# Kernel optimization log

Measured on AMD Instinct MI355X. Metric: run time of the kernel, lower is better.

Reference implementation:

```python
import jax, jax.numpy as jnp
import numpy as np

DIM = 2048
N_HEADS = 32
N_KV_HEADS = 8
HEAD_DIM = DIM // N_HEADS
ROPE_BASE = 10000.0
BATCH = 2
SEQ = 2048


def _rope_cos_sin(seq_len, dtype=jnp.float32):
    inv_freq = 1.0 / (ROPE_BASE ** (jnp.arange(0, HEAD_DIM, 2, dtype=jnp.float32) / HEAD_DIM))
    pos = jnp.arange(seq_len, dtype=jnp.float32)
    freqs = pos[:, None] * inv_freq[None, :]  # (seq, head_dim/2)
    return jnp.cos(freqs).astype(dtype), jnp.sin(freqs).astype(dtype)


def _apply_rope(x, cos, sin):
    # x: (b, h, s, d); cos/sin: (s, d/2). Interleaved (even/odd) RoPE.
    cos = cos[None, None, :, :]
    sin = sin[None, None, :, :]
    x_even = x[..., ::2]
    x_odd = x[..., 1::2]
    rot_even = x_even * cos - x_odd * sin
    rot_odd = x_even * sin + x_odd * cos
    out = jnp.stack((rot_even, rot_odd), axis=-1)
    return out.reshape(x.shape)


def setup_inputs() -> dict:
    key = jax.random.key(0)
    ks = jax.random.split(key, 5)
    s = 0.02
    return {
        "x": jax.random.normal(ks[0], (BATCH, SEQ, DIM), dtype=jnp.float32),
        "wq": jax.random.normal(ks[1], (DIM, N_HEADS * HEAD_DIM), dtype=jnp.float32) * s,
        "wk": jax.random.normal(ks[2], (DIM, N_KV_HEADS * HEAD_DIM), dtype=jnp.float32) * s,
        "wv": jax.random.normal(ks[3], (DIM, N_KV_HEADS * HEAD_DIM), dtype=jnp.float32) * s,
        "wo": jax.random.normal(ks[4], (DIM, DIM), dtype=jnp.float32) * s,
    }


def reference(x, wq, wk, wv, wo):
    b, s, _ = x.shape
    q = (x @ wq).reshape(b, s, N_HEADS, HEAD_DIM).transpose(0, 2, 1, 3)
    k = (x @ wk).reshape(b, s, N_KV_HEADS, HEAD_DIM).transpose(0, 2, 1, 3)
    v = (x @ wv).reshape(b, s, N_KV_HEADS, HEAD_DIM).transpose(0, 2, 1, 3)
    cos, sin = _rope_cos_sin(s, x.dtype)
    q = _apply_rope(q, cos, sin)
    k = _apply_rope(k, cos, sin)
    rep = N_HEADS // N_KV_HEADS
    if rep > 1:
        k = jnp.repeat(k, rep, axis=1)
        v = jnp.repeat(v, rep, axis=1)
    scores = jnp.einsum("bhqd,bhkd->bhqk", q, k) / (HEAD_DIM ** 0.5)
    causal = jnp.tril(jnp.ones((s, s), dtype=bool))
    scores = jnp.where(causal[None, None], scores, -jnp.inf)
    probs = jax.nn.softmax(scores, axis=-1)
    out = jnp.einsum("bhqk,bhkd->bhqd", probs, v)
    out = out.transpose(0, 2, 1, 3).reshape(b, s, DIM)
    return out @ wo
```

## Files before the change

### kernel.cpp

```cpp
#include <hip/hip_runtime.h>
#include <stdint.h>

#define DIM   2048
#define NH    32
#define NKV   8
#define HD    64
#define BATCH 2
#define SEQ   2048

typedef __attribute__((ext_vector_type(8))) short  short8;
typedef __attribute__((ext_vector_type(4))) short  short4v;
typedef __attribute__((ext_vector_type(4))) float  f32x4;

#if __has_builtin(__builtin_amdgcn_exp2f)
#define EXP2(x) __builtin_amdgcn_exp2f(x)
#else
#define EXP2(x) exp2f(x)
#endif

static __device__ __forceinline__ short f2bf(float f) {
  union { float f; uint32_t u; } v; v.f = f;
  uint32_t r = v.u + 0x7FFFu + ((v.u >> 16) & 1u);
  return (short)(r >> 16);
}

static __device__ __forceinline__ uint32_t cvtpk_bf16(float lo, float hi) {
  uint32_t r;
  asm("v_cvt_pk_bf16_f32 %0, %1, %2" : "=v"(r) : "v"(lo), "v"(hi));
  return r;
}

#define GLD16(gp, lp) __builtin_amdgcn_global_load_lds(                      \
    (__attribute__((address_space(1))) void*)(void*)(gp),                    \
    (__attribute__((address_space(3))) void*)(lp), 16, 0, 0)

#define QSCALE 0.1803368801111244f


__global__ void cvt_x_kernel(const float* __restrict__ in, short* __restrict__ out, int n4) {
  int i = blockIdx.x * blockDim.x + threadIdx.x;
  if (i < n4) {
    f32x4 v = *reinterpret_cast<const f32x4*>(in + (size_t)i * 4);
    short4v o;
    o.x = f2bf(v.x); o.y = f2bf(v.y); o.z = f2bf(v.z); o.w = f2bf(v.w);
    *reinterpret_cast<short4v*>(out + (size_t)i * 4) = o;
  }
}

__global__ void transpose_bf_kernel(const float* __restrict__ in, short* __restrict__ out,
                                    int R, int C) {
  __shared__ float t[32][33];
  int c0 = blockIdx.x * 32, r0 = blockIdx.y * 32;
  int tx = threadIdx.x, ty = threadIdx.y;
#pragma unroll
  for (int j = 0; j < 32; j += 8)
    t[ty + j][tx] = in[(size_t)(r0 + ty + j) * C + c0 + tx];
  __syncthreads();
#pragma unroll
  for (int j = 0; j < 32; j += 8)
    out[(size_t)(c0 + ty + j) * R + r0 + tx] = f2bf(t[tx][ty + j]);
}

__global__ void rope_tab_kernel(float* __restrict__ ct, float* __restrict__ st) {
  int i = blockIdx.x * blockDim.x + threadIdx.x;
  if (i < SEQ * 32) {
    int pos = i >> 5, f = i & 31;
    float inv = powf(10000.0f, -(float)f / 32.0f);
    float th = (float)pos * inv;
    ct[i] = cosf(th);
    st[i] = sinf(th);
  }
}


template <int BM, int BN, int WN>
__device__ __forceinline__ void gemm_8ph(const short* __restrict__ A,
                                         const short* __restrict__ Bt,
                                         int m0, int n0,
                                         short* __restrict__ As,
                                         short* __restrict__ Bs,
                                         f32x4 (&acc)[BM / ((8 / WN) * 16)][BN / (WN * 16)]) {
  constexpr int WM = 8 / WN;
  constexpr int MREP = BM / (WM * 16);
  constexpr int NREP = BN / (WN * 16);
  constexpr int MR2 = MREP / 2, NR2 = NREP / 2;
  constexpr int APASS = BM / 64, BPASS = BN / 64;
  constexpr int ABUF = BM * 64, BBUF = BN * 64;
  constexpr int NT = DIM / 64;

  const int tid = threadIdx.x;
  const int w = tid >> 6, l = tid & 63;
  const int lg = l >> 4, lr = l & 15;
  const int wr = w / WN, wc = w % WN;
  const int srow = tid >> 3;
  const int su2 = (tid & 7) ^ (srow & 7);
  const short* pA0 = A + (size_t)(m0 + srow) * DIM + su2 * 8;
  const short* pB0 = Bt + (size_t)(n0 + srow) * DIM + su2 * 8;

  auto stageA = [&](int t, int buf) {
#pragma unroll
    for (int p = 0; p < APASS; ++p)
      GLD16(pA0 + (size_t)p * 64 * DIM + t * 64, As + buf * ABUF + p * 4096 + w * 512);
  };
  auto stageB = [&](int t, int buf) {
#pragma unroll
    for (int p = 0; p < BPASS; ++p)
      GLD16(pB0 + (size_t)p * 64 * DIM + t * 64, Bs + buf * BBUF + p * 4096 + w * 512);
  };

  short8 af[MR2][2], bf0[NR2][2], bf1[NR2][2];

  auto readA = [&](int mh, const short* base) {
#pragma unroll
    for (int i = 0; i < MR2; ++i) {
      const int row = wr * (MREP * 16) + (mh * MR2 + i) * 16 + lr;
#pragma unroll
      for (int kk = 0; kk < 2; ++kk)
        af[i][kk] = *(const short8*)&base[row * 64 + (((kk * 4 + lg) ^ (row & 7)) << 3)];
    }
  };
  auto readB = [&](short8 (&bf)[NR2][2], int nh, const short* base) {
#pragma unroll
    for (int j = 0; j < NR2; ++j) {
      const int row = wc * (NREP * 16) + (nh * NR2 + j) * 16 + lr;
#pragma unroll
      for (int kk = 0; kk < 2; ++kk)
        bf[j][kk] = *(const short8*)&base[row * 64 + (((kk * 4 + lg) ^ (row & 7)) << 3)];
    }
  };
  auto mmaQ = [&](short8 (&bf)[NR2][2], int mh, int nh) {
    __builtin_amdgcn_s_setprio(1);
#pragma unroll
    for (int i = 0; i < MR2; ++i)
#pragma unroll
      for (int j = 0; j < NR2; ++j)
#pragma unroll
        for (int kk = 0; kk < 2; ++kk)
          acc[mh * MR2 + i][nh * NR2 + j] = __builtin_amdgcn_mfma_f32_16x16x32_bf16(
              af[i][kk], bf[j][kk], acc[mh * MR2 + i][nh * NR2 + j], 0, 0, 0);
    __builtin_amdgcn_s_setprio(0);
  };

#define PH_SYNC do { __builtin_amdgcn_s_barrier();                           \
    asm volatile("s_waitcnt lgkmcnt(0)" ::: "memory");                       \
    __builtin_amdgcn_sched_barrier(0); } while (0)

  stageA(0, 0);
  stageB(0, 0);
  asm volatile("s_waitcnt vmcnt(0)" ::: "memory");
  __builtin_amdgcn_s_barrier();

  for (int t = 0; t < NT; ++t) {
    const int cur = t & 1;
    const short* ab = As + cur * ABUF;
    const short* bb = Bs + cur * BBUF;
    const bool more = (t + 1 < NT);
    readA(0, ab);
    readB(bf0, 0, bb);
    if (more) stageA(t + 1, cur ^ 1);
    PH_SYNC;
    mmaQ(bf0, 0, 0);
    __builtin_amdgcn_s_barrier();
    readB(bf1, 1, bb);
    if (more) stageB(t + 1, cur ^ 1);
    PH_SYNC;
    mmaQ(bf1, 0, 1);
    __builtin_amdgcn_s_barrier();
    readA(1, ab);
    PH_SYNC;
    mmaQ(bf0, 1, 0);
    __builtin_amdgcn_s_barrier();
    PH_SYNC;
    mmaQ(bf1, 1, 1);
    asm volatile("s_waitcnt vmcnt(0)" ::: "memory");
    __builtin_amdgcn_s_barrier();
  }
#undef PH_SYNC
}

__device__ __forceinline__ int2 xcd_swizzle(int nwg) {
  int id = blockIdx.y * gridDim.x + blockIdx.x;
  int swz = (id & 7) * (nwg >> 3) + (id >> 3);
  return make_int2(swz % gridDim.x, swz / gridDim.x);
}

__global__ void __launch_bounds__(512, 2)
gemm_qkv_kernel(const short* __restrict__ A,
                const short* __restrict__ wqt, const short* __restrict__ wkt,
                const short* __restrict__ wvt,
                short* __restrict__ q_ws, short* __restrict__ k_ws, short* __restrict__ v_ws,
                const float* __restrict__ ct, const float* __restrict__ st) {
  __shared__ __align__(16) short As[2 * 256 * 64];
  __shared__ __align__(16) short Bs[2 * 256 * 64];
  int2 bxy = xcd_swizzle(12 * 16);
  const int n0g = bxy.x * 256;
  const int m0 = bxy.y * 256;
  int mode, n0;
  const short* Bt;
  short* outp;
  if (n0g < 2048)      { mode = 1; Bt = wqt; n0 = n0g;        outp = q_ws; }
  else if (n0g < 2560) { mode = 2; Bt = wkt; n0 = n0g - 2048; outp = k_ws; }
  else                 { mode = 3; Bt = wvt; n0 = n0g - 2560; outp = v_ws; }

  f32x4 acc[8][4] = {};
  gemm_8ph<256, 256, 4>(A, Bt, m0, n0, As, Bs, acc);

  const int tid = threadIdx.x;
  const int w = tid >> 6, l = tid & 63;
  const int lg = l >> 4, lr = l & 15;
  const int wr = w >> 2, wc = w & 3;
  const int mrow0 = m0 + wr * 128;
  const int ncol0 = n0 + wc * 64;
#pragma unroll
  for (int mt = 0; mt < 8; ++mt)
#pragma unroll
    for (int nt = 0; nt < 4; ++nt)
#pragma unroll
      for (int i = 0; i < 4; ++i) {
        int m = mrow0 + mt * 16 + lg * 4 + i;
        int n = ncol0 + nt * 16 + lr;
        float v = acc[mt][nt][i];
        int b = m >> 11, s = m & (SEQ - 1);
        int h = n >> 6, d = n & 63;
        if (mode == 3) {
          outp[((size_t)(b * NKV + h) * HD + d) * SEQ + s] = f2bf(v);
        } else {
          float p = __shfl_xor(v, 1);
          float cs = ct[(s << 5) + (d >> 1)];
          float sn = st[(s << 5) + (d >> 1)];
          float r = ((d & 1) == 0) ? (v * cs - p * sn) : (p * sn + v * cs);
          if (mode == 1) {
            r *= QSCALE;
            outp[((size_t)(b * NH + h) * SEQ + s) * HD + d] = f2bf(r);
          } else {
            outp[((size_t)(b * NKV + h) * SEQ + s) * HD + d] = f2bf(r);
          }
        }
      }
}

__global__ void __launch_bounds__(512, 2)
gemm_o_kernel(const short* __restrict__ A, const short* __restrict__ Bt,
              float* __restrict__ out) {
  __shared__ __align__(16) short As[2 * 128 * 64];
  __shared__ __align__(16) short Bs[2 * 256 * 64];
  int2 bxy = xcd_swizzle(8 * 32);
  const int m0 = bxy.y * 128, n0 = bxy.x * 256;
  f32x4 acc[4][4] = {};
  gemm_8ph<128, 256, 4>(A, Bt, m0, n0, As, Bs, acc);
  const int tid = threadIdx.x;
  const int w = tid >> 6, l = tid & 63;
  const int lg = l >> 4, lr = l & 15;
  const int wr = w >> 2, wc = w & 3;
#pragma unroll
  for (int mt = 0; mt < 4; ++mt)
#pragma unroll
    for (int nt = 0; nt < 4; ++nt)
#pragma unroll
      for (int i = 0; i < 4; ++i) {
        int m = m0 + wr * 64 + mt * 16 + lg * 4 + i;
        int n = n0 + wc * 64 + nt * 16 + lr;
        out[(size_t)m * DIM + n] = acc[mt][nt][i];
      }
}

__global__ void __launch_bounds__(256, 3)
attn_fwd_kernel(const short* __restrict__ Q, const short* __restrict__ K,
                const short* __restrict__ V, short* __restrict__ O) {
  __shared__ __align__(16) short Ks[3][4096];
  __shared__ __align__(16) short Vs[3][4096];
  const int tid = threadIdx.x;
  const int w = tid >> 6, l = tid & 63;
  const int lg = l >> 4, lr = l & 15;
  const int h = blockIdx.y;
  const int b = blockIdx.z;
  const int kvh = h >> 2;
  const int lh = lg >> 1, sub = (lg & 1) << 2;

  const short* kbase = K + (size_t)(b * NKV + kvh) * SEQ * HD;
  const short* vbase = V + (size_t)(b * NKV + kvh) * HD * SEQ;

  const int c1 = tid + 256;
  const int r0 = tid >> 3, e0 = ((tid & 7) ^ (r0 & 7)) << 3;
  const int r1 = c1 >> 3, e1 = ((c1 & 7) ^ (r1 & 7)) << 3;

  short8 ones;
#pragma unroll
  for (int i = 0; i < 8; ++i) ones[i] = (short)0x3F80;

#define ASTAGE(kvt, KB, VB) do { const int kv_ = (kvt) * 64;                  \
    GLD16(kbase + (size_t)(kv_ + r0) * HD + e0, (KB) + w * 512);              \
    GLD16(kbase + (size_t)(kv_ + r1) * HD + e1, (KB) + 2048 + w * 512);       \
    GLD16(vbase + (size_t)r0 * SEQ + kv_ + e0, (VB) + w * 512);               \
    GLD16(vbase + (size_t)r1 * SEQ + kv_ + e1, (VB) + 2048 + w * 512); } while (0)

  for (int qi = 0; qi < 2; ++qi) {
    const int qblk = (qi == 0) ? (int)blockIdx.x : (31 - (int)blockIdx.x);
    const int q0 = qblk * 64;
    const int qrow = q0 + w * 16 + lr;

    const short* qptr = Q + ((size_t)(b * NH + h) * SEQ + qrow) * HD;
    short8 qf0 = *(const short8*)(qptr + (lg << 3));
    short8 qf1 = *(const short8*)(qptr + 32 + (lg << 3));

    float m_run = 0.f;
    f32x4 oacc[4] = {};
    f32x4 lacc = {};

    short* kb0 = Ks[0]; short* kb1 = Ks[1]; short* kb2 = Ks[2];
    short* vb0 = Vs[0]; short* vb1 = Vs[1]; short* vb2 = Vs[2];

    ASTAGE(0, kb0, vb0);
    if (qblk >= 1) ASTAGE(1, kb1, vb1);

    for (int t = 0; t <= qblk; ++t) {
      if (t < qblk) asm volatile("s_waitcnt vmcnt(4)" ::: "memory");
      else          asm volatile("s_waitcnt vmcnt(0)" ::: "memory");
      __builtin_amdgcn_s_barrier();
      __builtin_amdgcn_sched_barrier(0);
      if (t + 2 <= qblk) ASTAGE(t + 2, kb2, vb2);

      const short* ks = kb0;
      const short* vs = vb0;
      const int kv0 = t * 64;

      short8 ka[4][2];
#pragma unroll
      for (int t4 = 0; t4 < 4; ++t4) {
        int row = t4 * 16 + lr, rx = row & 7;
        ka[t4][0] = *(const short8*)&ks[row * 64 + ((lg ^ rx) << 3)];
        ka[t4][1] = *(const short8*)&ks[row * 64 + (((4 + lg) ^ rx) << 3)];
      }
      short8 vbf[4][2];
#pragma unroll
      for (int nt = 0; nt < 4; ++nt) {
        int row = nt * 16 + lr, rx = row & 7;
#pragma unroll
        for (int ks_ = 0; ks_ < 2; ++ks_) {
          union { short8 s8; short4v hh[2]; } u;
          u.hh[0] = *(const short4v*)&vs[row * 64 + (((4 * ks_ + lh) ^ rx) << 3) + sub];
          u.hh[1] = *(const short4v*)&vs[row * 64 + (((4 * ks_ + 2 + lh) ^ rx) << 3) + sub];
          vbf[nt][ks_] = u.s8;
        }
      }

      f32x4 sacc[4];
      {
        f32x4 seed;
        seed[0] = -m_run; seed[1] = -m_run; seed[2] = -m_run; seed[3] = -m_run;
        __builtin_amdgcn_s_setprio(1);
#pragma unroll
        for (int t4 = 0; t4 < 4; ++t4) {
          f32x4 z = __builtin_amdgcn_mfma_f32_16x16x32_bf16(ka[t4][0], qf0, seed, 0, 0, 0);
          sacc[t4] = __builtin_amdgcn_mfma_f32_16x16x32_bf16(ka[t4][1], qf1, z, 0, 0, 0);
        }
        __builtin_amdgcn_s_setprio(0);
      }

      if (t == qblk) {
#pragma unroll
        for (int t4 = 0; t4 < 4; ++t4)
#pragma unroll
          for (int i = 0; i < 4; ++i)
            if (kv0 + t4 * 16 + lg * 4 + i > qrow) sacc[t4][i] = -__builtin_inff();
      }

      float a0 = fmaxf(fmaxf(sacc[0][0], sacc[0][1]), sacc[0][2]);
      float a1 = fmaxf(fmaxf(sacc[0][3], sacc[1][0]), sacc[1][1]);
      float a2 = fmaxf(fmaxf(sacc[1][2], sacc[1][3]), sacc[2][0]);
      float a3 = fmaxf(fmaxf(sacc[2][1], sacc[2][2]), sacc[2][3]);
      float a4 = fmaxf(fmaxf(sacc[3][0], sacc[3][1]), sacc[3][2]);
      float tm = fmaxf(fmaxf(fmaxf(a0, a1), a2), fmaxf(fmaxf(a3, a4), sacc[3][3]));
      tm = fmaxf(tm, __shfl_xor(tm, 16));
      tm = fmaxf(tm, __shfl_xor(tm, 32));

      if (!__all(tm <= 12.0f)) {
        float d = fmaxf(tm, 0.f);
        float alpha = EXP2(-d);
        float av0 = __shfl(alpha, (lg << 2));
        float av1 = __shfl(alpha, (lg << 2) | 1);
        float av2 = __shfl(alpha, (lg << 2) | 2);
        float av3 = __shfl(alpha, (lg << 2) | 3);
#pragma unroll
        for (int nt = 0; nt < 4; ++nt) {
          oacc[nt][0] *= av0; oacc[nt][1] *= av1;
          oacc[nt][2] *= av2; oacc[nt][3] *= av3;
        }
        lacc[0] *= av0; lacc[1] *= av1; lacc[2] *= av2; lacc[3] *= av3;
        m_run += d;
#pragma unroll
        for (int t4 = 0; t4 < 4; ++t4)
#pragma unroll
          for (int i = 0; i < 4; ++i) sacc[t4][i] -= d;
      }

      union { short8 s8; uint32_t u[4]; } pa0, pa1;
      pa0.u[0] = cvtpk_bf16(EXP2(sacc[0][0]), EXP2(sacc[0][1]));
      pa0.u[1] = cvtpk_bf16(EXP2(sacc[0][2]), EXP2(sacc[0][3]));
      pa0.u[2] = cvtpk_bf16(EXP2(sacc[1][0]), EXP2(sacc[1][1]));
      pa0.u[3] = cvtpk_bf16(EXP2(sacc[1][2]), EXP2(sacc[1][3]));
      pa1.u[0] = cvtpk_bf16(EXP2(sacc[2][0]), EXP2(sacc[2][1]));
      pa1.u[1] = cvtpk_bf16(EXP2(sacc[2][2]), EXP2(sacc[2][3]));
      pa1.u[2] = cvtpk_bf16(EXP2(sacc[3][0]), EXP2(sacc[3][1]));
      pa1.u[3] = cvtpk_bf16(EXP2(sacc[3][2]), EXP2(sacc[3][3]));

      __builtin_amdgcn_s_setprio(1);
#pragma unroll
      for (int nt = 0; nt < 4; ++nt) {
        oacc[nt] = __builtin_amdgcn_mfma_f32_16x16x32_bf16(pa0.s8, vbf[nt][0], oacc[nt], 0, 0, 0);
        oacc[nt] = __builtin_amdgcn_mfma_f32_16x16x32_bf16(pa1.s8, vbf[nt][1], oacc[nt], 0, 0, 0);
      }
      lacc = __builtin_amdgcn_mfma_f32_16x16x32_bf16(pa0.s8, ones, lacc, 0, 0, 0);
      lacc = __builtin_amdgcn_mfma_f32_16x16x32_bf16(pa1.s8, ones, lacc, 0, 0, 0);
      __builtin_amdgcn_s_setprio(0);

      short* tk = kb0; kb0 = kb1; kb1 = kb2; kb2 = tk;
      short* tv = vb0; vb0 = vb1; vb1 = vb2; vb2 = tv;
    }

    float linv0 = 1.f / lacc[0], linv1 = 1.f / lacc[1];
    float linv2 = 1.f / lacc[2], linv3 = 1.f / lacc[3];
#pragma unroll
    for (int nt = 0; nt < 4; ++nt) {
      int d = nt * 16 + lr;
      int qb = q0 + w * 16 + lg * 4;
      O[(size_t)(b * SEQ + qb + 0) * DIM + h * HD + d] = f2bf(oacc[nt][0] * linv0);
      O[(size_t)(b * SEQ + qb + 1) * DIM + h * HD + d] = f2bf(oacc[nt][1] * linv1);
      O[(size_t)(b * SEQ + qb + 2) * DIM + h * HD + d] = f2bf(oacc[nt][2] * linv2);
      O[(size_t)(b * SEQ + qb + 3) * DIM + h * HD + d] = f2bf(oacc[nt][3] * linv3);
    }
    __syncthreads();
  }
#undef ASTAGE
}


extern "C" void kernel_launch(void* const* d_in, const int* in_sizes, int n_in,
                              void* d_out, int out_size, void* d_ws, size_t ws_size,
                              hipStream_t stream) {
  const float* x  = (const float*)d_in[0];
  const float* wq = (const float*)d_in[1];
  const float* wk = (const float*)d_in[2];
  const float* wv = (const float*)d_in[3];
  const float* wo = (const float*)d_in[4];
  float* out = (float*)d_out;
  char* ws = (char*)d_ws;

  short* x_bf  = (short*)(ws + 0);
  short* attn  = (short*)(ws + 0);
  short* q_ws  = (short*)(ws + 16777216);
  short* k_ws  = (short*)(ws + 33554432);
  short* v_ws  = (short*)(ws + 37748736);
  short* wq_t  = (short*)(ws + 41943040);
  short* wo_t  = (short*)(ws + 41943040);
  short* wk_t  = (short*)(ws + 50331648);
  short* wv_t  = (short*)(ws + 52428800);
  float* ct    = (float*)(ws + 54525952);
  float* st    = (float*)(ws + 54788096);
  (void)ws_size; (void)in_sizes; (void)n_in; (void)out_size;

  dim3 tb(32, 8);
  cvt_x_kernel<<<8192, 256, 0, stream>>>(x, x_bf, 2097152);
  transpose_bf_kernel<<<dim3(64, 64), tb, 0, stream>>>(wq, wq_t, DIM, 2048);
  transpose_bf_kernel<<<dim3(16, 64), tb, 0, stream>>>(wk, wk_t, DIM, 512);
  transpose_bf_kernel<<<dim3(16, 64), tb, 0, stream>>>(wv, wv_t, DIM, 512);
  rope_tab_kernel<<<256, 256, 0, stream>>>(ct, st);

  gemm_qkv_kernel<<<dim3(12, 16), 512, 0, stream>>>(x_bf, wq_t, wk_t, wv_t,
                                                    q_ws, k_ws, v_ws, ct, st);

  attn_fwd_kernel<<<dim3(16, 32, 2), 256, 0, stream>>>(q_ws, k_ws, v_ws, attn);

  transpose_bf_kernel<<<dim3(64, 64), tb, 0, stream>>>(wo, wo_t, DIM, 2048);
  gemm_o_kernel<<<dim3(8, 32), 512, 0, stream>>>(attn, wo_t, out);
}
```

Measured before the change: 230.5 us.

## Split GEMM tile staging into halves with partial vmcnt waits

Tile prefetch in the shared bf16 GEMM mainloop is now issued as two halves, each covering part of the A and B passes, instead of all of A then all of B. The full `vmcnt(0)` drain at the end of each iteration becomes partial `vmcnt(N)` waits placed mid-iteration, so later loads can still be in flight while MFMA work runs. Some barriers are dropped or moved. This relies on every half being fully landed before any warp reads it, which depends on how warp row ownership lines up with pass halves; if it does not, warps can read stale shared-memory data.

```diff
diff --git a/kernel.cpp b/kernel.cpp
--- a/kernel.cpp
+++ b/kernel.cpp
@@ -33,6 +33,15 @@
 #define GLD16(gp, lp) __builtin_amdgcn_global_load_lds(                      \
     (__attribute__((address_space(1))) void*)(void*)(gp),                    \
     (__attribute__((address_space(3))) void*)(lp), 16, 0, 0)
+
+template <int N>
+__device__ __forceinline__ void vmwait() {
+  if constexpr (N == 0)      asm volatile("s_waitcnt vmcnt(0)" ::: "memory");
+  else if constexpr (N == 3) asm volatile("s_waitcnt vmcnt(3)" ::: "memory");
+  else if constexpr (N == 4) asm volatile("s_waitcnt vmcnt(4)" ::: "memory");
+  else if constexpr (N == 6) asm volatile("s_waitcnt vmcnt(6)" ::: "memory");
+  else                       asm volatile("s_waitcnt vmcnt(8)" ::: "memory");
+}
 
 #define QSCALE 0.1803368801111244f
 
@@ -85,6 +94,8 @@
   constexpr int NREP = BN / (WN * 16);
   constexpr int MR2 = MREP / 2, NR2 = NREP / 2;
   constexpr int APASS = BM / 64, BPASS = BN / 64;
+  constexpr int AH = APASS / 2, BH = BPASS / 2;
+  constexpr int VMN = AH + BH;
   constexpr int ABUF = BM * 64, BBUF = BN * 64;
   constexpr int NT = DIM / 64;
 
@@ -97,14 +108,12 @@
   const short* pA0 = A + (size_t)(m0 + srow) * DIM + su2 * 8;
   const short* pB0 = Bt + (size_t)(n0 + srow) * DIM + su2 * 8;
 
-  auto stageA = [&](int t, int buf) {
-#pragma unroll
-    for (int p = 0; p < APASS; ++p)
+  auto stageG = [&](int t, int buf, int half) {
+#pragma unroll
+    for (int p = half * AH; p < half * AH + AH; ++p)
       GLD16(pA0 + (size_t)p * 64 * DIM + t * 64, As + buf * ABUF + p * 4096 + w * 512);
-  };
-  auto stageB = [&](int t, int buf) {
-#pragma unroll
-    for (int p = 0; p < BPASS; ++p)
+#pragma unroll
+    for (int p = half * BH; p < half * BH + BH; ++p)
       GLD16(pB0 + (size_t)p * 64 * DIM + t * 64, Bs + buf * BBUF + p * 4096 + w * 512);
   };
 
@@ -141,41 +150,42 @@
     __builtin_amdgcn_s_setprio(0);
   };
 
-#define PH_SYNC do { __builtin_amdgcn_s_barrier();                           \
-    asm volatile("s_waitcnt lgkmcnt(0)" ::: "memory");                       \
+#define LGKM0 do { asm volatile("s_waitcnt lgkmcnt(0)" ::: "memory");        \
     __builtin_amdgcn_sched_barrier(0); } while (0)
-
-  stageA(0, 0);
-  stageB(0, 0);
-  asm volatile("s_waitcnt vmcnt(0)" ::: "memory");
-  __builtin_amdgcn_s_barrier();
+#define BAR __builtin_amdgcn_s_barrier()
+
+  stageG(0, 0, 0);
+  stageG(0, 0, 1);
+  vmwait<VMN>();
+  BAR;
 
   for (int t = 0; t < NT; ++t) {
-    const int cur = t & 1;
-    const short* ab = As + cur * ABUF;
-    const short* bb = Bs + cur * BBUF;
+    const int b = t & 1;
+    const short* ab = As + b * ABUF;
+    const short* bb = Bs + b * BBUF;
     const bool more = (t + 1 < NT);
     readA(0, ab);
     readB(bf0, 0, bb);
-    if (more) stageA(t + 1, cur ^ 1);
-    PH_SYNC;
+    if (more) stageG(t + 1, b ^ 1, 0);
+    BAR; LGKM0;
     mmaQ(bf0, 0, 0);
-    __builtin_amdgcn_s_barrier();
+    if (more) vmwait<VMN>(); else vmwait<0>();
+    BAR;
     readB(bf1, 1, bb);
-    if (more) stageB(t + 1, cur ^ 1);
-    PH_SYNC;
+    if (more) stageG(t + 1, b ^ 1, 1);
+    BAR; LGKM0;
     mmaQ(bf1, 0, 1);
-    __builtin_amdgcn_s_barrier();
+    BAR;
     readA(1, ab);
-    PH_SYNC;
+    BAR; LGKM0;
     mmaQ(bf0, 1, 0);
-    __builtin_amdgcn_s_barrier();
-    PH_SYNC;
+    vmwait<VMN>();
+    BAR;
     mmaQ(bf1, 1, 1);
-    asm volatile("s_waitcnt vmcnt(0)" ::: "memory");
-    __builtin_amdgcn_s_barrier();
+    BAR;
   }
-#undef PH_SYNC
+#undef LGKM0
+#undef BAR
 }
 
 __device__ __forceinline__ int2 xcd_swizzle(int nwg) {
```

Result: no change. 231.0 us (+0.2%).
